# Kernel optimization log

Measured on AMD Instinct MI355X. Metric: run time of the kernel, lower is better.

## Reference

```python
import jax, jax.numpy as jnp
import numpy as np

HIDDEN = 2560
NUM_HEADS = 32
HEAD_DIM = HIDDEN // NUM_HEADS          # 80
ROTARY_DIM = int(0.4 * HEAD_DIM)        # 32 (partial rotary)
ROPE_BASE = 10000.0
SCALE = HEAD_DIM ** -0.5


def _apply_partial_rope(x, pos):
    # x: [B, S, H, D], pos: [B, S] int. NeoX-style rotation on first ROTARY_DIM dims.
    half = ROTARY_DIM // 2
    inv_freq = 1.0 / (ROPE_BASE ** (jnp.arange(half, dtype=jnp.float32) / half))
    ang = pos.astype(jnp.float32)[..., None] * inv_freq      # [B, S, half]
    cos = jnp.cos(ang)[:, :, None, :]                        # [B, S, 1, half]
    sin = jnp.sin(ang)[:, :, None, :]
    x1 = x[..., :half]
    x2 = x[..., half:ROTARY_DIM]
    x_pass = x[..., ROTARY_DIM:]
    o1 = x1 * cos - x2 * sin
    o2 = x2 * cos + x1 * sin
    return jnp.concatenate([o1, o2, x_pass], axis=-1)


def setup_inputs() -> dict:
    key = jax.random.key(0)
    ks = jax.random.split(key, 5)
    B, S = 2, 2048
    hidden_states = jax.random.normal(ks[0], (B, S, HIDDEN), dtype=jnp.float32)
    position_ids = jnp.tile(jnp.arange(S, dtype=jnp.int32)[None, :], (B, 1))
    w_std = HIDDEN ** -0.5
    Wqkv = jax.random.normal(ks[1], (HIDDEN, 3 * HIDDEN), dtype=jnp.float32) * w_std
    bqkv = jax.random.normal(ks[2], (3 * HIDDEN,), dtype=jnp.float32) * 0.02
    Wd = jax.random.normal(ks[3], (HIDDEN, HIDDEN), dtype=jnp.float32) * w_std
    bd = jax.random.normal(ks[4], (HIDDEN,), dtype=jnp.float32) * 0.02
    return {"position_ids": position_ids, "hidden_states": hidden_states,
            "Wqkv": Wqkv, "bqkv": bqkv, "Wd": Wd, "bd": bd}


def reference(position_ids, hidden_states, Wqkv, bqkv, Wd, bd):
    B, S, _ = hidden_states.shape
    qkv = hidden_states @ Wqkv + bqkv                         # [B, S, 3*HIDDEN]
    q, k, v = jnp.split(qkv, 3, axis=-1)
    q = q.reshape(B, S, NUM_HEADS, HEAD_DIM)
    k = k.reshape(B, S, NUM_HEADS, HEAD_DIM)
    v = v.reshape(B, S, NUM_HEADS, HEAD_DIM)
    q = _apply_partial_rope(q, position_ids)
    k = _apply_partial_rope(k, position_ids)
    # causal self-attention (RadixAttention prefill with empty prefix)
    scores = jnp.einsum('bqhd,bkhd->bhqk', q, k) * SCALE      # [B, H, S, S]
    causal = jnp.tril(jnp.ones((S, S), dtype=bool))
    scores = jnp.where(causal[None, None], scores, jnp.finfo(scores.dtype).min)
    probs = jax.nn.softmax(scores, axis=-1)
    attn = jnp.einsum('bhqk,bkhd->bqhd', probs, v).reshape(B, S, HIDDEN)
    return attn @ Wd + bd
```

## Files before the change

kernel.cpp:

```cpp
#include <hip/hip_runtime.h>

#define HIDDEN 2560
#define NHEADS 32
#define HDIM 80
#define DPAD 96
#define SEQ 2048
#define M_TOK 4096
#define N_QKV 7680
#define ATT_SCALE 0.11180339887498949f

typedef __attribute__((ext_vector_type(4))) float f32x4;
typedef __attribute__((ext_vector_type(16))) float f32x16;
typedef __attribute__((ext_vector_type(4))) int i32x4;
typedef __attribute__((ext_vector_type(8))) short bf16x8;
typedef __attribute__((ext_vector_type(8))) unsigned short ushort8;

#define BAR() asm volatile("s_barrier" ::: "memory")

__device__ __forceinline__ unsigned short f2bf(float f) {
    unsigned int u = __float_as_uint(f);
    u += 0x7FFFu + ((u >> 16) & 1u);
    return (unsigned short)(u >> 16);
}
__device__ __forceinline__ float bf2f(unsigned short h) {
    return __uint_as_float(((unsigned int)h) << 16);
}

__device__ __forceinline__ void async_copy16(unsigned short* lds, const unsigned short* g) {
    __builtin_amdgcn_global_load_lds((const __attribute__((address_space(1))) void*)g,
                                     (__attribute__((address_space(3))) void*)lds, 16, 0, 0);
}

__device__ __forceinline__ int cvt_pk_bf16(float lo, float hi) {
    int d;
    asm("v_cvt_pk_bf16_f32 %0, %1, %2" : "=v"(d) : "v"(lo), "v"(hi));
    return d;
}

__global__ __launch_bounds__(256) void cvt_kernel(const float* __restrict__ in,
                                                  unsigned short* __restrict__ out, int n8) {
    int i = blockIdx.x * 256 + threadIdx.x;
    if (i >= n8) return;
    const float4* p = (const float4*)in + (size_t)i * 2;
    float4 a = p[0], b = p[1];
    ushort8 o;
    o[0] = f2bf(a.x); o[1] = f2bf(a.y); o[2] = f2bf(a.z); o[3] = f2bf(a.w);
    o[4] = f2bf(b.x); o[5] = f2bf(b.y); o[6] = f2bf(b.z); o[7] = f2bf(b.w);
    *((ushort8*)out + i) = o;
}

__global__ __launch_bounds__(256) void transpose_kernel(const float* __restrict__ in,
                                                        unsigned short* __restrict__ out,
                                                        int R, int C) {
    __shared__ unsigned short tile[64][66];
    const int r0 = blockIdx.y * 64, c0 = blockIdx.x * 64;
    const int t = threadIdx.x;
#pragma unroll
    for (int rep = 0; rep < 16; ++rep) {
        int idx = rep * 256 + t;
        int i = idx >> 6, j = idx & 63;
        tile[i][j] = f2bf(in[(size_t)(r0 + i) * C + (c0 + j)]);
    }
    __syncthreads();
#pragma unroll
    for (int rep = 0; rep < 16; ++rep) {
        int idx = rep * 256 + t;
        int j = idx >> 6, i = idx & 63;
        out[(size_t)(c0 + j) * R + (r0 + i)] = tile[i][j];
    }
}

template <int OUT_BF16>
__global__ __launch_bounds__(512, 2) void gemm256(const unsigned short* __restrict__ A,
                                                  const unsigned short* __restrict__ Bt,
                                                  const float* __restrict__ bias,
                                                  void* __restrict__ C,
                                                  int M, int N, int K) {
    __shared__ __align__(16) unsigned short S[4][16384];
    const int t = threadIdx.x;
    const int lane = t & 63, wid = t >> 6;
    const int wm = wid >> 2, wn = wid & 3;
    const int l15 = lane & 15, lhi = lane >> 4;

    const int cpx = (int)gridDim.x >> 3;
    const int wg = ((int)blockIdx.x % 8) * cpx + ((int)blockIdx.x >> 3);
    const int bm = (wg & 15) * 256;
    const int bn = (wg >> 4) * 256;

    int srow[2], scol[2];
#pragma unroll
    for (int c = 0; c < 2; ++c) {
        int idx = t + c * 512;
        srow[c] = idx >> 2;
        scol[c] = ((idx & 3) ^ ((srow[c] >> 1) & 3)) * 8;
    }
    const unsigned short* Abase = A + (size_t)bm * K;
    const unsigned short* Bbase = Bt + (size_t)bn * K;
    const int NT = K >> 6;

    int aoff[8], boff[4];
#pragma unroll
    for (int i = 0; i < 8; ++i) {
        int r = wm * 128 + i * 16 + l15;
        aoff[i] = r * 32 + ((lhi ^ ((r >> 1) & 3)) * 8);
    }
#pragma unroll
    for (int f = 0; f < 4; ++f) {
        int r = wn * 64 + f * 16 + l15;
        boff[f] = 8192 + r * 32 + ((lhi ^ ((r >> 1) & 3)) * 8);
    }

    f32x4 acc[8][4] = {};

#define STAGE_A(J) { const int j_ = (J); unsigned short* d = &S[j_ & 3][0];            \
    _Pragma("unroll")                                                                  \
    for (int c = 0; c < 2; ++c)                                                        \
        async_copy16(d + (t + c * 512) * 8,                                            \
                     Abase + (size_t)srow[c] * K + j_ * 32 + scol[c]); }
#define STAGE_B(J) { const int j_ = (J); unsigned short* d = &S[j_ & 3][8192];         \
    _Pragma("unroll")                                                                  \
    for (int c = 0; c < 2; ++c)                                                        \
        async_copy16(d + (t + c * 512) * 8,                                            \
                     Bbase + (size_t)srow[c] * K + j_ * 32 + scol[c]); }

#define PERIOD(J, VM, DOSTAGE) {                                                       \
    const int jp_ = (J);                                                               \
    asm volatile("s_waitcnt vmcnt(" #VM ")" ::: "memory");                             \
    BAR();                                                                             \
    const unsigned short* sl = &S[jp_ & 3][0];                                         \
    if (DOSTAGE) STAGE_A(jp_ + 3);                                                     \
    bf16x8 bq[4], afr[4];                                                              \
    _Pragma("unroll")                                                                  \
    for (int f = 0; f < 4; ++f) bq[f] = *(const bf16x8*)(sl + boff[f]);                \
    _Pragma("unroll")                                                                  \
    for (int i = 0; i < 4; ++i) afr[i] = *(const bf16x8*)(sl + aoff[i]);               \
    __builtin_amdgcn_s_setprio(1);                                                     \
    _Pragma("unroll")                                                                  \
    for (int i = 0; i < 4; ++i)                                                        \
        _Pragma("unroll")                                                              \
        for (int f = 0; f < 4; ++f)                                                    \
            acc[i][f] = __builtin_amdgcn_mfma_f32_16x16x32_bf16(afr[i], bq[f],         \
                                                                acc[i][f], 0, 0, 0);   \
    __builtin_amdgcn_s_setprio(0);                                                     \
    if (DOSTAGE) STAGE_B(jp_ + 3);                                                     \
    _Pragma("unroll")                                                                  \
    for (int i = 0; i < 4; ++i) afr[i] = *(const bf16x8*)(sl + aoff[4 + i]);           \
    __builtin_amdgcn_s_setprio(1);                                                     \
    _Pragma("unroll")                                                                  \
    for (int i = 0; i < 4; ++i)                                                        \
        _Pragma("unroll")                                                              \
        for (int f = 0; f < 4; ++f)                                                    \
            acc[4 + i][f] = __builtin_amdgcn_mfma_f32_16x16x32_bf16(afr[i], bq[f],     \
                                                                    acc[4 + i][f],     \
                                                                    0, 0, 0);          \
    __builtin_amdgcn_s_setprio(0); }

    STAGE_A(0); STAGE_B(0);
    STAGE_A(1); STAGE_B(1);
    STAGE_A(2); STAGE_B(2);

    for (int T = 0; T < NT - 2; ++T) {
        PERIOD(2 * T, 8, 1);
        PERIOD(2 * T + 1, 8, 1);
    }
    PERIOD(2 * NT - 4, 8, 1);
    PERIOD(2 * NT - 3, 8, 0);
    PERIOD(2 * NT - 2, 4, 0);
    PERIOD(2 * NT - 1, 0, 0);

#undef PERIOD
#undef STAGE_A
#undef STAGE_B

#pragma unroll
    for (int f = 0; f < 4; ++f) {
        const int col = bn + wn * 64 + f * 16 + l15;
        const float bv = bias[col];
#pragma unroll
        for (int i = 0; i < 8; ++i) {
            const int row0 = bm + wm * 128 + i * 16 + lhi * 4;
#pragma unroll
            for (int r = 0; r < 4; ++r) {
                float v = acc[i][f][r] + bv;
                if (OUT_BF16)
                    ((unsigned short*)C)[(size_t)(row0 + r) * N + col] = f2bf(v);
                else
                    ((float*)C)[(size_t)(row0 + r) * N + col] = v;
            }
        }
    }
}

__global__ __launch_bounds__(256) void pack_rope_kernel(const unsigned short* __restrict__ qkv,
                                                        const int* __restrict__ pos_ids,
                                                        unsigned short* __restrict__ Qb,
                                                        unsigned short* __restrict__ Kb,
                                                        unsigned short* __restrict__ Vt) {
    int g = blockIdx.x * 256 + threadIdx.x;
    int s = g & (SEQ - 1);
    int bh = g >> 11;
    int b = bh >> 5;
    int h = bh & 31;
    int m = b * SEQ + s;
    const unsigned short* base = qkv + (size_t)m * N_QKV + h * HDIM;
    unsigned short* Qrow = Qb + ((size_t)bh * SEQ + s) * DPAD;
    unsigned short* Krow = Kb + ((size_t)bh * SEQ + s) * DPAD;
    unsigned short* Vcol = Vt + (size_t)bh * HDIM * SEQ + s;

    float pos = (float)pos_ids[m];
    float qv[32], kv[32];
#pragma unroll
    for (int c = 0; c < 4; ++c) {
        ushort8 qc = *(const ushort8*)(base + c * 8);
        ushort8 kc = *(const ushort8*)(base + HIDDEN + c * 8);
#pragma unroll
        for (int j = 0; j < 8; ++j) {
            qv[c * 8 + j] = bf2f(qc[j]);
            kv[c * 8 + j] = bf2f(kc[j]);
        }
    }
#pragma unroll
    for (int d = 0; d < 16; ++d) {
        float inv = __expf(-(float)d * 0.5756462732485115f);
        float ang = pos * inv;
        float sn, cs;
        __sincosf(ang, &sn, &cs);
        float qcs = cs * ATT_SCALE, qsn = sn * ATT_SCALE;
        float x1 = qv[d], x2 = qv[d + 16];
        qv[d] = x1 * qcs - x2 * qsn;
        qv[d + 16] = x2 * qcs + x1 * qsn;
        x1 = kv[d]; x2 = kv[d + 16];
        kv[d] = x1 * cs - x2 * sn;
        kv[d + 16] = x2 * cs + x1 * sn;
    }
#pragma unroll
    for (int c = 0; c < 4; ++c) {
        ushort8 qo, ko;
#pragma unroll
        for (int j = 0; j < 8; ++j) {
            qo[j] = f2bf(qv[c * 8 + j]);
            ko[j] = f2bf(kv[c * 8 + j]);
        }
        *(ushort8*)(Qrow + c * 8) = qo;
        *(ushort8*)(Krow + c * 8) = ko;
    }
#pragma unroll
    for (int c = 4; c < 10; ++c) {
        ushort8 qc = *(const ushort8*)(base + c * 8);
        ushort8 qo;
#pragma unroll
        for (int j = 0; j < 8; ++j) qo[j] = f2bf(bf2f(qc[j]) * ATT_SCALE);
        *(ushort8*)(Qrow + c * 8) = qo;
        *(ushort8*)(Krow + c * 8) = *(const ushort8*)(base + HIDDEN + c * 8);
    }
    ushort8 z = {0, 0, 0, 0, 0, 0, 0, 0};
    *(ushort8*)(Qrow + 80) = z;
    *(ushort8*)(Qrow + 88) = z;
    *(ushort8*)(Krow + 80) = z;
    *(ushort8*)(Krow + 88) = z;
#pragma unroll
    for (int d = 0; d < HDIM; ++d) Vcol[(size_t)d * SEQ] = base[2 * HIDDEN + d];
}

__global__ __launch_bounds__(512) void flash_kernel(const unsigned short* __restrict__ Qb,
                                                    const unsigned short* __restrict__ Kb,
                                                    const unsigned short* __restrict__ Vt,
                                                    unsigned short* __restrict__ attn) {
    __shared__ __align__(16) unsigned short Klds[64 * 128];
    __shared__ __align__(16) unsigned short Vlds[96 * 64];

    const int bh = blockIdx.x;
    const int qb = 7 - (int)blockIdx.y;
    const int q0b = qb * 256;
    const int nkt = 4 * qb + 4;
    const int t = threadIdx.x;
    const int lane = t & 63, wid = t >> 6;
    const int l31 = lane & 31, h = lane >> 5, l7 = lane & 7;
    const int q0w = q0b + wid * 32;
    const int swz = l7 << 3;

    const unsigned short* Kbase = Kb + (size_t)bh * SEQ * DPAD;
    const unsigned short* Vbase = Vt + (size_t)bh * HDIM * SEQ;

    bf16x8 qf[6];
    {
        const unsigned short* Qrow = Qb + ((size_t)bh * SEQ + q0w + l31) * DPAD + h * 8;
#pragma unroll
        for (int dc = 0; dc < 6; ++dc) qf[dc] = *(const bf16x8*)(Qrow + dc * 16);
    }

    ((int*)Vlds)[2560 + t] = 0;

    f32x16 acc0 = {}, acc1 = {}, acc2 = {};
    float mrow = -1e30f, lrow = 0.f;

    const int kidx1 = 512 + t;
    const int kr0 = t / 12, kc0 = t % 12;
    const int kr1 = kidx1 / 12, kc1 = kidx1 % 12;
    const int vr0 = t >> 3, vc0 = t & 7;
    const int vr1 = (512 + t) >> 3, vc1 = t & 7;
    const int kd0 = kr0 * 128 + ((kc0 * 8) ^ ((kr0 & 7) << 3));
    const int kd1 = kr1 * 128 + ((kc1 * 8) ^ ((kr1 & 7) << 3));
    const int vd0 = vr0 * 64 + ((vc0 * 8) ^ ((vr0 & 7) << 3));
    const int vd1 = vr1 * 64 + ((vc1 * 8) ^ ((vr1 & 7) << 3));

    ushort8 kreg0, kreg1, vreg0, vreg1;
    kreg0 = *(const ushort8*)(Kbase + (size_t)t * 8);
    if (t < 256) kreg1 = *(const ushort8*)(Kbase + (size_t)kidx1 * 8);
    vreg0 = *(const ushort8*)(Vbase + (size_t)vr0 * SEQ + vc0 * 8);
    if (t < 128) vreg1 = *(const ushort8*)(Vbase + (size_t)vr1 * SEQ + vc1 * 8);

    for (int kt = 0; kt < nkt; ++kt) {
        const int k0 = kt * 64;
        __syncthreads();
        *(ushort8*)(Klds + kd0) = kreg0;
        if (t < 256) *(ushort8*)(Klds + kd1) = kreg1;
        *(ushort8*)(Vlds + vd0) = vreg0;
        if (t < 128) *(ushort8*)(Vlds + vd1) = vreg1;
        __syncthreads();
        if (kt + 1 < nkt) {
            const int kn = k0 + 64;
            kreg0 = *(const ushort8*)(Kbase + (size_t)kn * DPAD + (size_t)t * 8);
            if (t < 256) kreg1 = *(const ushort8*)(Kbase + (size_t)kn * DPAD + (size_t)kidx1 * 8);
            vreg0 = *(const ushort8*)(Vbase + (size_t)vr0 * SEQ + kn + vc0 * 8);
            if (t < 128) vreg1 = *(const ushort8*)(Vbase + (size_t)vr1 * SEQ + kn + vc1 * 8);
        }
        if (k0 > q0w + 31) continue;

        f32x16 s0 = {}, s1 = {};
        __builtin_amdgcn_s_setprio(1);
#pragma unroll
        for (int dc = 0; dc < 6; ++dc) {
            const int co = (dc * 16 + h * 8) ^ swz;
            bf16x8 ka = *(const bf16x8*)(Klds + l31 * 128 + co);
            bf16x8 kb2 = *(const bf16x8*)(Klds + (32 + l31) * 128 + co);
            s0 = __builtin_amdgcn_mfma_f32_32x32x16_bf16(ka, qf[dc], s0, 0, 0, 0);
            s1 = __builtin_amdgcn_mfma_f32_32x32x16_bf16(kb2, qf[dc], s1, 0, 0, 0);
        }
        __builtin_amdgcn_s_setprio(0);

        const int qg = q0w + l31;
        if (k0 + 63 > q0w) {
#pragma unroll
            for (int r = 0; r < 16; ++r) {
                const int kg = k0 + (r & 3) + 8 * (r >> 2) + 4 * h;
                if (kg > qg) s0[r] = -2e30f;
                if (kg + 32 > qg) s1[r] = -2e30f;
            }
        }
        float pmax = s0[0];
#pragma unroll
        for (int r = 1; r < 16; ++r) pmax = fmaxf(pmax, s0[r]);
#pragma unroll
        for (int r = 0; r < 16; ++r) pmax = fmaxf(pmax, s1[r]);
        pmax = fmaxf(pmax, __shfl_xor(pmax, 32, 64));
        if (!__all(pmax <= mrow + 8.0f)) {
            float mnew = fmaxf(mrow, pmax);
            float scl = __expf(mrow - mnew);
            mrow = mnew;
            lrow *= scl;
#pragma unroll
            for (int r = 0; r < 16; ++r) {
                float sq = __shfl(scl, (r & 3) + 8 * (r >> 2) + 4 * h, 64);
                acc0[r] *= sq; acc1[r] *= sq; acc2[r] *= sq;
            }
        }
        float ps = 0.f;
#pragma unroll
        for (int r = 0; r < 16; ++r) { s0[r] = __expf(s0[r] - mrow); ps += s0[r]; }
#pragma unroll
        for (int r = 0; r < 16; ++r) { s1[r] = __expf(s1[r] - mrow); ps += s1[r]; }
        lrow += ps + __shfl_xor(ps, 32, 64);
        i32x4 af[2][2];
#pragma unroll
        for (int ks = 0; ks < 2; ++ks) {
            const f32x16& sv = ks ? s1 : s0;
            int pk0[2], pk1[2], pk2[2], pk3[2];
#pragma unroll
            for (int i = 0; i < 2; ++i) {
                pk0[i] = cvt_pk_bf16(sv[2 * i], sv[2 * i + 1]);
                pk1[i] = cvt_pk_bf16(sv[4 + 2 * i], sv[5 + 2 * i]);
                pk2[i] = cvt_pk_bf16(sv[8 + 2 * i], sv[9 + 2 * i]);
                pk3[i] = cvt_pk_bf16(sv[12 + 2 * i], sv[13 + 2 * i]);
            }
#pragma unroll
            for (int i = 0; i < 2; ++i) {
                const int o0 = __shfl_xor(pk0[i], 32, 64);
                const int o1 = __shfl_xor(pk1[i], 32, 64);
                af[ks][0][i]     = h ? o1     : pk0[i];
                af[ks][0][2 + i] = h ? pk1[i] : o0;
                const int o2 = __shfl_xor(pk2[i], 32, 64);
                const int o3 = __shfl_xor(pk3[i], 32, 64);
                af[ks][1][i]     = h ? o3     : pk2[i];
                af[ks][1][2 + i] = h ? pk3[i] : o2;
            }
        }
        __builtin_amdgcn_s_setprio(1);
#pragma unroll
        for (int ds = 0; ds < 3; ++ds) {
            f32x16& ac = ds == 0 ? acc0 : (ds == 1 ? acc1 : acc2);
            const int vrow = (ds * 32 + l31) * 64;
#pragma unroll
            for (int ks = 0; ks < 2; ++ks)
#pragma unroll
                for (int kh = 0; kh < 2; ++kh) {
                    bf16x8 vb = *(const bf16x8*)(Vlds + vrow + ((ks * 32 + kh * 16 + h * 8) ^ swz));
                    bf16x8 pa = __builtin_bit_cast(bf16x8, af[ks][kh]);
                    ac = __builtin_amdgcn_mfma_f32_32x32x16_bf16(pa, vb, ac, 0, 0, 0);
                }
        }
        __builtin_amdgcn_s_setprio(0);
    }

    const int hh = bh & 31, b = bh >> 5;
    const float linv = 1.0f / lrow;
#pragma unroll
    for (int r = 0; r < 16; ++r) {
        const int ql = (r & 3) + 8 * (r >> 2) + 4 * h;
        const float lv = __shfl(linv, ql, 64);
        const int row = b * SEQ + q0b + wid * 32 + ql;
        unsigned short* orow = attn + (size_t)row * HIDDEN + hh * HDIM;
        orow[l31] = f2bf(acc0[r] * lv);
        orow[32 + l31] = f2bf(acc1[r] * lv);
        if (l31 < 16) orow[64 + l31] = f2bf(acc2[r] * lv);
    }
}

extern "C" void kernel_launch(void* const* d_in, const int* in_sizes, int n_in,
                              void* d_out, int out_size, void* d_ws, size_t ws_size,
                              hipStream_t stream) {
    const int* pos = (const int*)d_in[0];
    const float* hid = (const float*)d_in[1];
    const float* Wqkv = (const float*)d_in[2];
    const float* bqkv = (const float*)d_in[3];
    const float* Wd = (const float*)d_in[4];
    const float* bd = (const float*)d_in[5];
    float* out = (float*)d_out;
    char* ws = (char*)d_ws;

    unsigned short* WqkvT = (unsigned short*)(ws);
    unsigned short* WdT   = (unsigned short*)(ws + 39321600);
    unsigned short* Xbf   = (unsigned short*)(ws + 52428800);
    unsigned short* qkv   = (unsigned short*)(ws + 73400320);
    unsigned short* Qbuf  = (unsigned short*)(ws + 136314880);
    unsigned short* Kbuf  = (unsigned short*)(ws + 161480704);
    unsigned short* Vt    = (unsigned short*)(ws + 186646528);
    unsigned short* attnb = Xbf;

    cvt_kernel<<<(M_TOK * HIDDEN / 8 + 255) / 256, 256, 0, stream>>>(hid, Xbf, M_TOK * HIDDEN / 8);
    transpose_kernel<<<dim3(N_QKV / 64, HIDDEN / 64), 256, 0, stream>>>(Wqkv, WqkvT, HIDDEN, N_QKV);
    transpose_kernel<<<dim3(HIDDEN / 64, HIDDEN / 64), 256, 0, stream>>>(Wd, WdT, HIDDEN, HIDDEN);
    gemm256<1><<<(M_TOK / 256) * (N_QKV / 256), 512, 0, stream>>>(Xbf, WqkvT, bqkv, qkv,
                                                                  M_TOK, N_QKV, HIDDEN);
    pack_rope_kernel<<<(64 * SEQ) / 256, 256, 0, stream>>>(qkv, pos, Qbuf, Kbuf, Vt);
    flash_kernel<<<dim3(64, 8), 512, 0, stream>>>(Qbuf, Kbuf, Vt, attnb);
    gemm256<0><<<(M_TOK / 256) * (HIDDEN / 256), 512, 0, stream>>>(attnb, WdT, bd, out,
                                                                   M_TOK, HIDDEN, HIDDEN);
}
```

Baseline: 388.2 us.

## Restructure GEMM main loop into barrier-phased schedule overlapping LDS reads and async copies

Reorders each K-step period of the bf16 MFMA GEMM so that LDS fragment reads come before the barrier, and issues the next stage's async global-to-LDS copies between extra barriers. The second half's A fragments go into a separate register set (afr2). The vmcnt wait moves to the end of each period, and a dedicated last period drops the staging and the barriers. The aim is to hide LDS and global-load latency behind MFMA work, at the cost of more barriers per period and extra fragment registers.

```diff
diff --git a/kernel.cpp b/kernel.cpp
--- a/kernel.cpp
+++ b/kernel.cpp
@@ -125,15 +125,15 @@
 
 #define PERIOD(J, VM, DOSTAGE) {                                                       \
     const int jp_ = (J);                                                               \
-    asm volatile("s_waitcnt vmcnt(" #VM ")" ::: "memory");                             \
+    const unsigned short* sl = &S[jp_ & 3][0];                                         \
+    bf16x8 bq[4], afr[4], afr2[4];                                                     \
+    _Pragma("unroll")                                                                  \
+    for (int f = 0; f < 4; ++f) bq[f] = *(const bf16x8*)(sl + boff[f]);                \
+    _Pragma("unroll")                                                                  \
+    for (int i = 0; i < 4; ++i) afr[i] = *(const bf16x8*)(sl + aoff[i]);               \
+    if (DOSTAGE) STAGE_A(jp_ + 3);                                                     \
     BAR();                                                                             \
-    const unsigned short* sl = &S[jp_ & 3][0];                                         \
-    if (DOSTAGE) STAGE_A(jp_ + 3);                                                     \
-    bf16x8 bq[4], afr[4];                                                              \
-    _Pragma("unroll")                                                                  \
-    for (int f = 0; f < 4; ++f) bq[f] = *(const bf16x8*)(sl + boff[f]);                \
-    _Pragma("unroll")                                                                  \
-    for (int i = 0; i < 4; ++i) afr[i] = *(const bf16x8*)(sl + aoff[i]);               \
+    asm volatile("s_waitcnt lgkmcnt(0)" ::: "memory");                                 \
     __builtin_amdgcn_s_setprio(1);                                                     \
     _Pragma("unroll")                                                                  \
     for (int i = 0; i < 4; ++i)                                                        \
@@ -142,15 +142,46 @@
             acc[i][f] = __builtin_amdgcn_mfma_f32_16x16x32_bf16(afr[i], bq[f],         \
                                                                 acc[i][f], 0, 0, 0);   \
     __builtin_amdgcn_s_setprio(0);                                                     \
+    BAR();                                                                             \
+    _Pragma("unroll")                                                                  \
+    for (int i = 0; i < 4; ++i) afr2[i] = *(const bf16x8*)(sl + aoff[4 + i]);          \
     if (DOSTAGE) STAGE_B(jp_ + 3);                                                     \
-    _Pragma("unroll")                                                                  \
-    for (int i = 0; i < 4; ++i) afr[i] = *(const bf16x8*)(sl + aoff[4 + i]);           \
+    BAR();                                                                             \
+    asm volatile("s_waitcnt lgkmcnt(0)" ::: "memory");                                 \
     __builtin_amdgcn_s_setprio(1);                                                     \
     _Pragma("unroll")                                                                  \
     for (int i = 0; i < 4; ++i)                                                        \
         _Pragma("unroll")                                                              \
         for (int f = 0; f < 4; ++f)                                                    \
-            acc[4 + i][f] = __builtin_amdgcn_mfma_f32_16x16x32_bf16(afr[i], bq[f],     \
+            acc[4 + i][f] = __builtin_amdgcn_mfma_f32_16x16x32_bf16(afr2[i], bq[f],    \
+                                                                    acc[4 + i][f],     \
+                                                                    0, 0, 0);          \
+    __builtin_amdgcn_s_setprio(0);                                                     \
+    asm volatile("s_waitcnt vmcnt(" #VM ")" ::: "memory");                             \
+    BAR(); }
+
+#define PERIOD_LAST(J) {                                                               \
+    const int jp_ = (J);                                                               \
+    const unsigned short* sl = &S[jp_ & 3][0];                                         \
+    bf16x8 bq[4], afr[4], afr2[4];                                                     \
+    _Pragma("unroll")                                                                  \
+    for (int f = 0; f < 4; ++f) bq[f] = *(const bf16x8*)(sl + boff[f]);                \
+    _Pragma("unroll")                                                                  \
+    for (int i = 0; i < 4; ++i) afr[i] = *(const bf16x8*)(sl + aoff[i]);               \
+    _Pragma("unroll")                                                                  \
+    for (int i = 0; i < 4; ++i) afr2[i] = *(const bf16x8*)(sl + aoff[4 + i]);          \
+    __builtin_amdgcn_s_setprio(1);                                                     \
+    _Pragma("unroll")                                                                  \
+    for (int i = 0; i < 4; ++i)                                                        \
+        _Pragma("unroll")                                                              \
+        for (int f = 0; f < 4; ++f)                                                    \
+            acc[i][f] = __builtin_amdgcn_mfma_f32_16x16x32_bf16(afr[i], bq[f],         \
+                                                                acc[i][f], 0, 0, 0);   \
+    _Pragma("unroll")                                                                  \
+    for (int i = 0; i < 4; ++i)                                                        \
+        _Pragma("unroll")                                                              \
+        for (int f = 0; f < 4; ++f)                                                    \
+            acc[4 + i][f] = __builtin_amdgcn_mfma_f32_16x16x32_bf16(afr2[i], bq[f],    \
                                                                     acc[4 + i][f],     \
                                                                     0, 0, 0);          \
     __builtin_amdgcn_s_setprio(0); }
@@ -158,17 +189,20 @@
     STAGE_A(0); STAGE_B(0);
     STAGE_A(1); STAGE_B(1);
     STAGE_A(2); STAGE_B(2);
-
-    for (int T = 0; T < NT - 2; ++T) {
+    asm volatile("s_waitcnt vmcnt(8)" ::: "memory");
+    BAR();
+
+    for (int T = 0; T + 2 < NT; ++T) {
         PERIOD(2 * T, 8, 1);
         PERIOD(2 * T + 1, 8, 1);
     }
     PERIOD(2 * NT - 4, 8, 1);
-    PERIOD(2 * NT - 3, 8, 0);
-    PERIOD(2 * NT - 2, 4, 0);
-    PERIOD(2 * NT - 1, 0, 0);
+    PERIOD(2 * NT - 3, 4, 0);
+    PERIOD(2 * NT - 2, 0, 0);
+    PERIOD_LAST(2 * NT - 1);
 
 #undef PERIOD
+#undef PERIOD_LAST
 #undef STAGE_A
 #undef STAGE_B
 
```

Result: slower. 406.5 us (+4.7%).
